# Kernel optimization log

Measured on AMD Instinct MI355X. Metric: run time of the kernel, lower is better.

The kernel has to match this reference:

```python
import jax, jax.numpy as jnp
import numpy as np

N = 150000   # nodes
E = 600000   # edges
F_IN = 32    # node features
H = 128      # hidden_channels == MLP_neurons
G = 2048     # graphs in batch


def setup_inputs() -> dict:
    key = jax.random.key(0)
    ks = iter(jax.random.split(key, 40))
    inp = {}
    inp['x'] = jax.random.normal(next(ks), (N, F_IN), dtype=jnp.float32)
    inp['edge_index'] = jax.random.randint(next(ks), (2, E), 0, N)
    inp['batch'] = jnp.sort(jax.random.randint(next(ks), (N,), 0, G))
    # GINConv MLPs: Linear(in,H) ReLU Linear(H,H) ReLU Linear(H,H)
    for i, f_in in enumerate([F_IN, H, H]):
        s1 = 1.0 / np.sqrt(f_in)
        s2 = 1.0 / np.sqrt(H)
        inp[f'c{i}_w1'] = jax.random.uniform(next(ks), (f_in, H), minval=-s1, maxval=s1)
        inp[f'c{i}_b1'] = jnp.zeros((H,), jnp.float32)
        inp[f'c{i}_w2'] = jax.random.uniform(next(ks), (H, H), minval=-s2, maxval=s2)
        inp[f'c{i}_b2'] = jnp.zeros((H,), jnp.float32)
        inp[f'c{i}_w3'] = jax.random.uniform(next(ks), (H, H), minval=-s2, maxval=s2)
        inp[f'c{i}_b3'] = jnp.zeros((H,), jnp.float32)
    s = 1.0 / np.sqrt(H)
    inp['fc0_w'] = jax.random.uniform(next(ks), (H, H), minval=-s, maxval=s)
    inp['fc0_b'] = jnp.zeros((H,), jnp.float32)
    inp['fc1_w'] = jax.random.uniform(next(ks), (H, H), minval=-s, maxval=s)
    inp['fc1_b'] = jnp.zeros((H,), jnp.float32)
    inp['out_w'] = jax.random.uniform(next(ks), (H, 2), minval=-s, maxval=s)
    inp['out_b'] = jnp.zeros((2,), jnp.float32)
    return inp


def _gin_layer(x, edge_index, w1, b1, w2, b2, w3, b3):
    # GINConv with eps=0: h = MLP(x + sum_{j in N(i)} x_j)
    agg = jax.ops.segment_sum(x[edge_index[0]], edge_index[1], num_segments=N)
    h = x + agg
    h = jax.nn.relu(h @ w1 + b1)
    h = jax.nn.relu(h @ w2 + b2)
    h = h @ w3 + b3
    return jax.nn.relu(h)  # outer .relu() in forward


def reference(x, edge_index, batch,
              c0_w1, c0_b1, c0_w2, c0_b2, c0_w3, c0_b3,
              c1_w1, c1_b1, c1_w2, c1_b2, c1_w3, c1_b3,
              c2_w1, c2_b1, c2_w2, c2_b2, c2_w3, c2_b3,
              fc0_w, fc0_b, fc1_w, fc1_b, out_w, out_b):
    h = _gin_layer(x, edge_index, c0_w1, c0_b1, c0_w2, c0_b2, c0_w3, c0_b3)
    h = _gin_layer(h, edge_index, c1_w1, c1_b1, c1_w2, c1_b2, c1_w3, c1_b3)
    h = _gin_layer(h, edge_index, c2_w1, c2_b1, c2_w2, c2_b2, c2_w3, c2_b3)
    # global_mean_pool over graph ids
    sums = jax.ops.segment_sum(h, batch, num_segments=G)            # [G,H]
    cnts = jax.ops.segment_sum(jnp.ones((N,), h.dtype), batch, num_segments=G)
    g = sums / jnp.maximum(cnts, 1.0)[:, None]
    # classifier head (dropout is identity at inference)
    g = jax.nn.relu(g @ fc0_w + fc0_b)
    g = jax.nn.relu(g @ fc1_w + fc1_b)
    return g @ out_w + out_b  # [G,2]
```

## Files before the change

kernel.cpp:

```cpp
#include <hip/hip_runtime.h>
#include <hip/hip_bf16.h>

#define NN 150000
#define EE 600000
#define F_IN 32
#define HD 128
#define GG 2048
#define CAP 28
#define NP 150016

typedef __attribute__((ext_vector_type(8))) short bf16x8;
typedef __attribute__((ext_vector_type(4))) float f32x4;
typedef __attribute__((address_space(1))) const void g1void;
typedef __attribute__((address_space(3))) void l3void;

__device__ inline void split_bf16(float v, unsigned short& hi, unsigned short& lo) {
    __hip_bfloat16 h = __float2bfloat16(v);
    float hv = __bfloat162float(h);
    __hip_bfloat16 l = __float2bfloat16(v - hv);
    hi = *reinterpret_cast<unsigned short*>(&h);
    lo = *reinterpret_cast<unsigned short*>(&l);
}
__device__ inline unsigned short bf16_hi(float v) {
    __hip_bfloat16 h = __float2bfloat16(v);
    return *reinterpret_cast<unsigned short*>(&h);
}
__device__ inline float bf2f(unsigned short u) {
    union { unsigned int i; float f; } c;
    c.i = ((unsigned int)u) << 16;
    return c.f;
}

__global__ void init_zero(int* __restrict__ cnt_node, float* __restrict__ pooled) {
    int i = blockIdx.x * blockDim.x + threadIdx.x;
    if (i < NN) cnt_node[i] = 0;
    if (i < GG * HD) pooled[i] = 0.f;
}

__global__ void build_graph(const int* __restrict__ ei,
                            int* __restrict__ cnt_node,
                            int* __restrict__ bucket) {
    int e = blockIdx.x * blockDim.x + threadIdx.x;
    if (e >= EE) return;
    int src = ei[e];
    int dst = ei[EE + e];
    int slot = atomicAdd(&cnt_node[dst], 1);
    if (slot < CAP) bucket[dst * CAP + slot] = src;
}

struct PrepDesc { const float* src; unsigned short* dhi; unsigned short* dlo; int K; };
struct PrepArgs { PrepDesc d[9]; };

__global__ void prep_weights(PrepArgs pa) {
    PrepDesc de = pa.d[blockIdx.y];
    int total = de.K * HD;
    int KS = de.K >> 5;
    for (int idx = blockIdx.x * blockDim.x + threadIdx.x; idx < total;
         idx += gridDim.x * blockDim.x) {
        int k = idx / HD, h = idx - (idx / HD) * HD;
        unsigned short hi, lo;
        split_bf16(de.src[idx], hi, lo);
        int nt = h >> 4, m = h & 15;
        int ks = k >> 5, quad = (k >> 3) & 3, e = k & 7;
        int lane = quad * 16 + m;
        int pidx = ((nt * KS + ks) * 64 + lane) * 8 + e;
        de.dhi[pidx] = hi;
        de.dlo[pidx] = lo;
    }
}

template <int KS>
__device__ inline void stage_slice(const unsigned short* __restrict__ wh,
                                   const unsigned short* __restrict__ wl,
                                   int nt, unsigned short* dst, int wave, int lane) {
    if (KS == 4) {
        const unsigned short* gh = wh + nt * 2048 + wave * 512 + lane * 8;
        const unsigned short* gl = wl + nt * 2048 + wave * 512 + lane * 8;
        __builtin_amdgcn_global_load_lds((g1void*)gh, (l3void*)(dst + wave * 512), 16, 0, 0);
        __builtin_amdgcn_global_load_lds((g1void*)gl, (l3void*)(dst + 2048 + wave * 512), 16, 0, 0);
    } else {
        if (wave < 2) {
            const unsigned short* g = (wave == 0 ? wh : wl) + nt * 512 + lane * 8;
            __builtin_amdgcn_global_load_lds((g1void*)g, (l3void*)(dst + wave * 512), 16, 0, 0);
        }
    }
}

template <int K_IN, bool BF16IN, bool POOL>
__launch_bounds__(256, 2)
__global__ void gin_layer(const void* __restrict__ hin_,
                          const int* __restrict__ cnt_node,
                          const int* __restrict__ bucket,
                          const unsigned short* __restrict__ w1h, const unsigned short* __restrict__ w1l,
                          const float* __restrict__ b1,
                          const unsigned short* __restrict__ w2h, const unsigned short* __restrict__ w2l,
                          const float* __restrict__ b2,
                          const unsigned short* __restrict__ w3h, const unsigned short* __restrict__ w3l,
                          const float* __restrict__ b3,
                          unsigned short* __restrict__ out,
                          const int* __restrict__ batch,
                          float* __restrict__ pooled) {
    constexpr int KS1 = K_IN / 32;
    constexpr int UN = BF16IN ? 4 : (KS1 == 1 ? 8 : 2);
    __shared__ unsigned int shp[4][2][16][128];
    __shared__ unsigned short ldsW[2][4096];

    const int wave = threadIdx.x >> 6;
    const int lane = threadIdx.x & 63;
    const int m = lane & 15;
    const int quad = lane >> 4;
    const int nodeBase = blockIdx.x * 128 + wave * 32;

    const float* hf = (const float*)hin_;
    const unsigned short* hb = (const unsigned short*)hin_;

    bf16x8 ah[2][KS1], al[2][KS1];
#pragma unroll
    for (int s = 0; s < 2; s++) {
        int node = nodeBase + s * 16 + m;
        node = node < NN ? node : NN - 1;
        float ag[KS1][8];
        if (BF16IN) {
            const unsigned short* rs = hb + (size_t)node * K_IN + quad * 8;
#pragma unroll
            for (int ks = 0; ks < KS1; ks++) {
                bf16x8 v = *(const bf16x8*)(rs + ks * 32);
#pragma unroll
                for (int e = 0; e < 8; e++) ag[ks][e] = bf2f((unsigned short)v[e]);
            }
        } else {
            const float* rs = hf + (size_t)node * K_IN + quad * 8;
#pragma unroll
            for (int ks = 0; ks < KS1; ks++) {
                float4 v0 = *(const float4*)(rs + ks * 32);
                float4 v1 = *(const float4*)(rs + ks * 32 + 4);
                ag[ks][0] = v0.x; ag[ks][1] = v0.y; ag[ks][2] = v0.z; ag[ks][3] = v0.w;
                ag[ks][4] = v1.x; ag[ks][5] = v1.y; ag[ks][6] = v1.z; ag[ks][7] = v1.w;
            }
        }
        int cnt = cnt_node[node];
        cnt = cnt < CAP ? cnt : CAP;
        const int* b = bucket + (size_t)node * CAP;
        int i = 0;
        if (BF16IN) {
            for (; i + UN <= cnt; i += UN) {
                bf16x8 v[UN][KS1];
#pragma unroll
                for (int j = 0; j < UN; j++) {
                    const unsigned short* r = hb + (size_t)b[i + j] * K_IN + quad * 8;
#pragma unroll
                    for (int ks = 0; ks < KS1; ks++)
                        v[j][ks] = *(const bf16x8*)(r + ks * 32);
                }
#pragma unroll
                for (int ks = 0; ks < KS1; ks++)
#pragma unroll
                    for (int e = 0; e < 8; e++) {
                        float t01 = bf2f((unsigned short)v[0][ks][e]) +
                                    bf2f((unsigned short)v[1][ks][e]);
                        float t23 = bf2f((unsigned short)v[2][ks][e]) +
                                    bf2f((unsigned short)v[3][ks][e]);
                        ag[ks][e] += t01 + t23;
                    }
            }
            for (; i < cnt; i++) {
                const unsigned short* r = hb + (size_t)b[i] * K_IN + quad * 8;
#pragma unroll
                for (int ks = 0; ks < KS1; ks++) {
                    bf16x8 v = *(const bf16x8*)(r + ks * 32);
#pragma unroll
                    for (int e = 0; e < 8; e++) ag[ks][e] += bf2f((unsigned short)v[e]);
                }
            }
        } else {
            for (; i + UN <= cnt; i += UN) {
                float4 v0[UN][KS1], v1[UN][KS1];
#pragma unroll
                for (int j = 0; j < UN; j++) {
                    const float* r = hf + (size_t)b[i + j] * K_IN + quad * 8;
#pragma unroll
                    for (int ks = 0; ks < KS1; ks++) {
                        v0[j][ks] = *(const float4*)(r + ks * 32);
                        v1[j][ks] = *(const float4*)(r + ks * 32 + 4);
                    }
                }
#pragma unroll
                for (int ks = 0; ks < KS1; ks++) {
#pragma unroll
                    for (int e = 0; e < 4; e++) {
                        float s01 = (&v0[0][ks].x)[e] + (&v0[1][ks].x)[e];
                        float s23 = (&v0[2][ks].x)[e] + (&v0[3][ks].x)[e];
                        if (UN == 8) {
                            s01 += (&v0[4][ks].x)[e] + (&v0[5][ks].x)[e];
                            s23 += (&v0[6][ks].x)[e] + (&v0[7][ks].x)[e];
                        }
                        ag[ks][e] += s01 + s23;
                    }
#pragma unroll
                    for (int e = 0; e < 4; e++) {
                        float s01 = (&v1[0][ks].x)[e] + (&v1[1][ks].x)[e];
                        float s23 = (&v1[2][ks].x)[e] + (&v1[3][ks].x)[e];
                        if (UN == 8) {
                            s01 += (&v1[4][ks].x)[e] + (&v1[5][ks].x)[e];
                            s23 += (&v1[6][ks].x)[e] + (&v1[7][ks].x)[e];
                        }
                        ag[ks][e + 4] += s01 + s23;
                    }
                }
            }
            for (; i < cnt; i++) {
                const float* r = hf + (size_t)b[i] * K_IN + quad * 8;
#pragma unroll
                for (int ks = 0; ks < KS1; ks++) {
                    float4 v0 = *(const float4*)(r + ks * 32);
                    float4 v1 = *(const float4*)(r + ks * 32 + 4);
                    ag[ks][0] += v0.x; ag[ks][1] += v0.y; ag[ks][2] += v0.z; ag[ks][3] += v0.w;
                    ag[ks][4] += v1.x; ag[ks][5] += v1.y; ag[ks][6] += v1.z; ag[ks][7] += v1.w;
                }
            }
        }
#pragma unroll
        for (int ks = 0; ks < KS1; ks++) {
            bf16x8 vh, vl;
#pragma unroll
            for (int e = 0; e < 8; e++) {
                unsigned short hi, lo;
                split_bf16(ag[ks][e], hi, lo);
                vh[e] = (short)hi;
                vl[e] = (short)lo;
            }
            ah[s][ks] = vh;
            al[s][ks] = vl;
        }
    }

    bf16x8 a2h[2][4], a2l[2][4];
    const int fxm = (m & 7) << 2;

    stage_slice<KS1>(w1h, w1l, 0, ldsW[0], wave, lane);
    __syncthreads();
#pragma unroll 1
    for (int nt = 0; nt < 8; nt++) {
        int cur = nt & 1;
        if (nt < 7) stage_slice<KS1>(w1h, w1l, nt + 1, ldsW[cur ^ 1], wave, lane);
        bf16x8 bh[KS1], bl[KS1];
#pragma unroll
        for (int ks = 0; ks < KS1; ks++) {
            bh[ks] = *(const bf16x8*)&ldsW[cur][(ks * 64 + lane) * 8];
            bl[ks] = *(const bf16x8*)&ldsW[cur][KS1 * 512 + (ks * 64 + lane) * 8];
        }
        f32x4 c0 = {0.f, 0.f, 0.f, 0.f};
        f32x4 c1 = {0.f, 0.f, 0.f, 0.f};
#pragma unroll
        for (int ks = 0; ks < KS1; ks++) {
            c0 = __builtin_amdgcn_mfma_f32_16x16x32_bf16(ah[0][ks], bh[ks], c0, 0, 0, 0);
            c1 = __builtin_amdgcn_mfma_f32_16x16x32_bf16(ah[1][ks], bh[ks], c1, 0, 0, 0);
            c0 = __builtin_amdgcn_mfma_f32_16x16x32_bf16(al[0][ks], bh[ks], c0, 0, 0, 0);
            c1 = __builtin_amdgcn_mfma_f32_16x16x32_bf16(al[1][ks], bh[ks], c1, 0, 0, 0);
            c0 = __builtin_amdgcn_mfma_f32_16x16x32_bf16(ah[0][ks], bl[ks], c0, 0, 0, 0);
            c1 = __builtin_amdgcn_mfma_f32_16x16x32_bf16(ah[1][ks], bl[ks], c1, 0, 0, 0);
        }
        float bj = b1[nt * 16 + m];
#pragma unroll
        for (int r = 0; r < 4; r++) {
            int row = quad * 4 + r;
            int col = (nt * 16 + m) ^ ((row & 7) << 2);
            unsigned short hi, lo;
            split_bf16(fmaxf(c0[r] + bj, 0.f), hi, lo);
            shp[wave][0][row][col] = (unsigned int)hi | ((unsigned int)lo << 16);
            split_bf16(fmaxf(c1[r] + bj, 0.f), hi, lo);
            shp[wave][1][row][col] = (unsigned int)hi | ((unsigned int)lo << 16);
        }
        __syncthreads();
    }
    stage_slice<4>(w2h, w2l, 0, ldsW[0], wave, lane);
#pragma unroll
    for (int s = 0; s < 2; s++)
#pragma unroll
        for (int ks = 0; ks < 4; ks++) {
            const unsigned int* rowp = &shp[wave][s][m][0];
            int base = ks * 32 + quad * 8;
            uint4 wa = *(const uint4*)&rowp[base ^ fxm];
            uint4 wb = *(const uint4*)&rowp[(base + 4) ^ fxm];
            union { unsigned int u[4]; bf16x8 v; } ch, cl;
            ch.u[0] = __builtin_amdgcn_perm(wa.y, wa.x, 0x05040100u);
            ch.u[1] = __builtin_amdgcn_perm(wa.w, wa.z, 0x05040100u);
            ch.u[2] = __builtin_amdgcn_perm(wb.y, wb.x, 0x05040100u);
            ch.u[3] = __builtin_amdgcn_perm(wb.w, wb.z, 0x05040100u);
            cl.u[0] = __builtin_amdgcn_perm(wa.y, wa.x, 0x07060302u);
            cl.u[1] = __builtin_amdgcn_perm(wa.w, wa.z, 0x07060302u);
            cl.u[2] = __builtin_amdgcn_perm(wb.y, wb.x, 0x07060302u);
            cl.u[3] = __builtin_amdgcn_perm(wb.w, wb.z, 0x07060302u);
            a2h[s][ks] = ch.v;
            a2l[s][ks] = cl.v;
        }
    __syncthreads();

#pragma unroll 1
    for (int nt = 0; nt < 8; nt++) {
        int cur = nt & 1;
        if (nt < 7) stage_slice<4>(w2h, w2l, nt + 1, ldsW[cur ^ 1], wave, lane);
        bf16x8 bh[4], bl[4];
#pragma unroll
        for (int ks = 0; ks < 4; ks++) {
            bh[ks] = *(const bf16x8*)&ldsW[cur][(ks * 64 + lane) * 8];
            bl[ks] = *(const bf16x8*)&ldsW[cur][2048 + (ks * 64 + lane) * 8];
        }
        f32x4 c0 = {0.f, 0.f, 0.f, 0.f};
        f32x4 c1 = {0.f, 0.f, 0.f, 0.f};
#pragma unroll
        for (int ks = 0; ks < 4; ks++) {
            c0 = __builtin_amdgcn_mfma_f32_16x16x32_bf16(a2h[0][ks], bh[ks], c0, 0, 0, 0);
            c1 = __builtin_amdgcn_mfma_f32_16x16x32_bf16(a2h[1][ks], bh[ks], c1, 0, 0, 0);
            c0 = __builtin_amdgcn_mfma_f32_16x16x32_bf16(a2l[0][ks], bh[ks], c0, 0, 0, 0);
            c1 = __builtin_amdgcn_mfma_f32_16x16x32_bf16(a2l[1][ks], bh[ks], c1, 0, 0, 0);
            c0 = __builtin_amdgcn_mfma_f32_16x16x32_bf16(a2h[0][ks], bl[ks], c0, 0, 0, 0);
            c1 = __builtin_amdgcn_mfma_f32_16x16x32_bf16(a2h[1][ks], bl[ks], c1, 0, 0, 0);
        }
        float bj = b2[nt * 16 + m];
#pragma unroll
        for (int r = 0; r < 4; r++) {
            int row = quad * 4 + r;
            int col = (nt * 16 + m) ^ ((row & 7) << 2);
            unsigned short hi, lo;
            split_bf16(fmaxf(c0[r] + bj, 0.f), hi, lo);
            shp[wave][0][row][col] = (unsigned int)hi | ((unsigned int)lo << 16);
            split_bf16(fmaxf(c1[r] + bj, 0.f), hi, lo);
            shp[wave][1][row][col] = (unsigned int)hi | ((unsigned int)lo << 16);
        }
        __syncthreads();
    }
    stage_slice<4>(w3h, w3l, 0, ldsW[0], wave, lane);
#pragma unroll
    for (int s = 0; s < 2; s++)
#pragma unroll
        for (int ks = 0; ks < 4; ks++) {
            const unsigned int* rowp = &shp[wave][s][m][0];
            int base = ks * 32 + quad * 8;
            uint4 wa = *(const uint4*)&rowp[base ^ fxm];
            uint4 wb = *(const uint4*)&rowp[(base + 4) ^ fxm];
            union { unsigned int u[4]; bf16x8 v; } ch, cl;
            ch.u[0] = __builtin_amdgcn_perm(wa.y, wa.x, 0x05040100u);
            ch.u[1] = __builtin_amdgcn_perm(wa.w, wa.z, 0x05040100u);
            ch.u[2] = __builtin_amdgcn_perm(wb.y, wb.x, 0x05040100u);
            ch.u[3] = __builtin_amdgcn_perm(wb.w, wb.z, 0x05040100u);
            cl.u[0] = __builtin_amdgcn_perm(wa.y, wa.x, 0x07060302u);
            cl.u[1] = __builtin_amdgcn_perm(wa.w, wa.z, 0x07060302u);
            cl.u[2] = __builtin_amdgcn_perm(wb.y, wb.x, 0x07060302u);
            cl.u[3] = __builtin_amdgcn_perm(wb.w, wb.z, 0x07060302u);
            a2h[s][ks] = ch.v;
            a2l[s][ks] = cl.v;
        }
    __syncthreads();

#pragma unroll 1
    for (int nt = 0; nt < 8; nt++) {
        int cur = nt & 1;
        if (nt < 7) stage_slice<4>(w3h, w3l, nt + 1, ldsW[cur ^ 1], wave, lane);
        bf16x8 bh[4], bl[4];
#pragma unroll
        for (int ks = 0; ks < 4; ks++) {
            bh[ks] = *(const bf16x8*)&ldsW[cur][(ks * 64 + lane) * 8];
            bl[ks] = *(const bf16x8*)&ldsW[cur][2048 + (ks * 64 + lane) * 8];
        }
        f32x4 c0 = {0.f, 0.f, 0.f, 0.f};
        f32x4 c1 = {0.f, 0.f, 0.f, 0.f};
#pragma unroll
        for (int ks = 0; ks < 4; ks++) {
            c0 = __builtin_amdgcn_mfma_f32_16x16x32_bf16(a2h[0][ks], bh[ks], c0, 0, 0, 0);
            c1 = __builtin_amdgcn_mfma_f32_16x16x32_bf16(a2h[1][ks], bh[ks], c1, 0, 0, 0);
            c0 = __builtin_amdgcn_mfma_f32_16x16x32_bf16(a2l[0][ks], bh[ks], c0, 0, 0, 0);
            c1 = __builtin_amdgcn_mfma_f32_16x16x32_bf16(a2l[1][ks], bh[ks], c1, 0, 0, 0);
            c0 = __builtin_amdgcn_mfma_f32_16x16x32_bf16(a2h[0][ks], bl[ks], c0, 0, 0, 0);
            c1 = __builtin_amdgcn_mfma_f32_16x16x32_bf16(a2h[1][ks], bl[ks], c1, 0, 0, 0);
        }
        float bj = b3[nt * 16 + m];
        if (POOL) {
            float* shf0 = (float*)&shp[wave][0][0][0];
            float* shf1 = (float*)&shp[wave][1][0][0];
#pragma unroll
            for (int r = 0; r < 4; r++) {
                int row = quad * 4 + r;
                int col = (nt * 16 + m) ^ ((row & 7) << 2);
                shf0[row * 128 + col] = fmaxf(c0[r] + bj, 0.f);
                shf1[row * 128 + col] = fmaxf(c1[r] + bj, 0.f);
            }
        } else {
            unsigned short* t0 = (unsigned short*)&shp[wave][0][0][0];
            unsigned short* t1 = (unsigned short*)&shp[wave][1][0][0];
#pragma unroll
            for (int r = 0; r < 4; r++) {
                int row = quad * 4 + r;
                int hh = nt * 16 + m;
                int w2 = (hh >> 1) ^ ((row & 7) << 2);
                t0[row * 256 + w2 * 2 + (hh & 1)] = bf16_hi(fmaxf(c0[r] + bj, 0.f));
                t1[row * 256 + w2 * 2 + (hh & 1)] = bf16_hi(fmaxf(c1[r] + bj, 0.f));
            }
        }
        __syncthreads();
    }

    if (POOL) {
#pragma unroll
        for (int h = 0; h < 2; h++) {
            float* shf = (float*)&shp[wave][h][0][0];
            int c0i = lane * 2;
            float run0 = 0.f, run1 = 0.f;
            int gp = -1;
            for (int rrow = 0; rrow < 16; rrow++) {
                int node = nodeBase + h * 16 + rrow;
                if (node >= NN) break;
                int g = batch[node];
                float2 xv = *(const float2*)&shf[rrow * 128 + (c0i ^ ((rrow & 7) << 2))];
                if (g != gp) {
                    if (gp >= 0) {
                        atomicAdd(&pooled[(size_t)gp * HD + c0i + 0], run0);
                        atomicAdd(&pooled[(size_t)gp * HD + c0i + 1], run1);
                    }
                    run0 = xv.x; run1 = xv.y; gp = g;
                } else {
                    run0 += xv.x; run1 += xv.y;
                }
            }
            if (gp >= 0) {
                atomicAdd(&pooled[(size_t)gp * HD + c0i + 0], run0);
                atomicAdd(&pooled[(size_t)gp * HD + c0i + 1], run1);
            }
        }
    } else {
#pragma unroll
        for (int s = 0; s < 2; s++) {
            unsigned short* sh16 = (unsigned short*)&shp[wave][s][0][0];
#pragma unroll
            for (int io = 0; io < 4; io++) {
                int row16 = io * 4 + quad;
                int wbase = (m * 4) ^ ((row16 & 7) << 2);
                int n2 = nodeBase + s * 16 + row16;
                bf16x8 v = *(const bf16x8*)&sh16[row16 * 256 + wbase * 2];
                if (n2 < NN) *(bf16x8*)&out[(size_t)n2 * HD + m * 8] = v;
            }
        }
    }
}

__device__ inline int lb_batch(const int* __restrict__ batch, int key) {
    int lo = 0, hi = NN;
    while (lo < hi) {
        int mid = (lo + hi) >> 1;
        if (batch[mid] < key) lo = mid + 1; else hi = mid;
    }
    return lo;
}

__launch_bounds__(128)
__global__ void head(const float* __restrict__ pooled, const int* __restrict__ batch,
                     const float* __restrict__ fc0_w, const float* __restrict__ fc0_b,
                     const float* __restrict__ fc1_w, const float* __restrict__ fc1_b,
                     const float* __restrict__ out_w, const float* __restrict__ out_b,
                     float* __restrict__ out) {
    int g = blockIdx.x;
    int j = threadIdx.x;
    __shared__ float s0[HD];
    __shared__ float s1[HD];
    int c = lb_batch(batch, g + 1) - lb_batch(batch, g);
    float cf = (float)(c > 1 ? c : 1);
    s0[j] = pooled[(size_t)g * HD + j] / cf;
    __syncthreads();

    float acc = fc0_b[j];
    for (int k = 0; k < HD; k += 4) {
        float4 hv = *(const float4*)&s0[k];
        acc = fmaf(hv.x, fc0_w[(k + 0) * HD + j], acc);
        acc = fmaf(hv.y, fc0_w[(k + 1) * HD + j], acc);
        acc = fmaf(hv.z, fc0_w[(k + 2) * HD + j], acc);
        acc = fmaf(hv.w, fc0_w[(k + 3) * HD + j], acc);
    }
    s1[j] = fmaxf(acc, 0.0f);
    __syncthreads();

    acc = fc1_b[j];
    for (int k = 0; k < HD; k += 4) {
        float4 hv = *(const float4*)&s1[k];
        acc = fmaf(hv.x, fc1_w[(k + 0) * HD + j], acc);
        acc = fmaf(hv.y, fc1_w[(k + 1) * HD + j], acc);
        acc = fmaf(hv.z, fc1_w[(k + 2) * HD + j], acc);
        acc = fmaf(hv.w, fc1_w[(k + 3) * HD + j], acc);
    }
    float v = fmaxf(acc, 0.0f);

    float p0 = v * out_w[j * 2 + 0];
    float p1 = v * out_w[j * 2 + 1];
    __syncthreads();
    s0[j] = p0;
    s1[j] = p1;
    __syncthreads();
    for (int off = 64; off >= 1; off >>= 1) {
        if (j < off) {
            s0[j] += s0[j + off];
            s1[j] += s1[j + off];
        }
        __syncthreads();
    }
    if (j == 0) {
        out[(size_t)g * 2 + 0] = s0[0] + out_b[0];
        out[(size_t)g * 2 + 1] = s1[0] + out_b[1];
    }
}

extern "C" void kernel_launch(void* const* d_in, const int* in_sizes, int n_in,
                              void* d_out, int out_size, void* d_ws, size_t ws_size,
                              hipStream_t stream) {
    const float* x     = (const float*)d_in[0];
    const int*   ei    = (const int*)d_in[1];
    const int*   batch = (const int*)d_in[2];
    const float* cw[3][6];
    for (int i = 0; i < 3; i++)
        for (int k = 0; k < 6; k++) cw[i][k] = (const float*)d_in[3 + 6 * i + k];
    const float* fc0_w = (const float*)d_in[21];
    const float* fc0_b = (const float*)d_in[22];
    const float* fc1_w = (const float*)d_in[23];
    const float* fc1_b = (const float*)d_in[24];
    const float* out_w = (const float*)d_in[25];
    const float* out_b = (const float*)d_in[26];
    float* out = (float*)d_out;

    char* ws = (char*)d_ws;
    size_t off = 0;
    auto carve = [&](size_t bytes) {
        void* p = ws + off;
        off += (bytes + 255) & ~(size_t)255;
        return p;
    };
    int*   cnt_node = (int*)carve((size_t)NN * 4);
    float* pooled   = (float*)carve((size_t)GG * HD * 4);
    int*   bucket   = (int*)carve((size_t)NN * CAP * 4);
    unsigned short* hA = (unsigned short*)carve((size_t)NP * HD * 2);
    unsigned short* hB = (unsigned short*)carve((size_t)NP * HD * 2);
    unsigned short* wHi[9];
    unsigned short* wLo[9];
    int wK[9] = {F_IN, HD, HD, HD, HD, HD, HD, HD, HD};
    for (int i = 0; i < 9; i++) {
        wHi[i] = (unsigned short*)carve((size_t)wK[i] * HD * 2);
        wLo[i] = (unsigned short*)carve((size_t)wK[i] * HD * 2);
    }
    (void)ws_size;

    init_zero<<<(GG * HD + 255) / 256, 256, 0, stream>>>(cnt_node, pooled);
    build_graph<<<(EE + 255) / 256, 256, 0, stream>>>(ei, cnt_node, bucket);

    PrepArgs pa;
    for (int l = 0; l < 3; l++)
        for (int s = 0; s < 3; s++) {
            int i = l * 3 + s;
            pa.d[i].src = cw[l][2 * s];
            pa.d[i].dhi = wHi[i];
            pa.d[i].dlo = wLo[i];
            pa.d[i].K = wK[i];
        }
    prep_weights<<<dim3(16, 9), 256, 0, stream>>>(pa);

    const int blocks = NP / 128;

    gin_layer<F_IN, false, false><<<blocks, 256, 0, stream>>>(x, cnt_node, bucket,
        wHi[0], wLo[0], cw[0][1], wHi[1], wLo[1], cw[0][3], wHi[2], wLo[2], cw[0][5],
        hA, batch, pooled);
    gin_layer<HD, true, false><<<blocks, 256, 0, stream>>>(hA, cnt_node, bucket,
        wHi[3], wLo[3], cw[1][1], wHi[4], wLo[4], cw[1][3], wHi[5], wLo[5], cw[1][5],
        hB, batch, pooled);
    gin_layer<HD, true, true><<<blocks, 256, 0, stream>>>(hB, cnt_node, bucket,
        wHi[6], wLo[6], cw[2][1], wHi[7], wLo[7], cw[2][3], wHi[8], wLo[8], cw[2][5],
        nullptr, batch, pooled);

    head<<<GG, 128, 0, stream>>>(pooled, batch, fc0_w, fc0_b, fc1_w, fc1_b, out_w, out_b, out);
}
```

Before: 474.6 us.

## Interleave neighbor gathers for both node halves and prefetch first weight slice earlier

The bf16 aggregation path now walks the neighbor lists of both 16-node halves together, two neighbors per step, using predicated loads that fall back to the node itself, so more independent gathers are in flight at once. The first W1 slice is staged into LDS before the gather so its load overlaps with aggregation. The fp32 path is specialised to KS1==1 with 8-way unrolling. The price is wasted loads when the two halves have different degrees, plus higher register pressure.

```diff
diff --git a/kernel.cpp b/kernel.cpp
--- a/kernel.cpp
+++ b/kernel.cpp
@@ -101,7 +101,6 @@
                           const int* __restrict__ batch,
                           float* __restrict__ pooled) {
     constexpr int KS1 = K_IN / 32;
-    constexpr int UN = BF16IN ? 4 : (KS1 == 1 ? 8 : 2);
     __shared__ unsigned int shp[4][2][16][128];
     __shared__ unsigned short ldsW[2][4096];
 
@@ -114,130 +113,128 @@
     const float* hf = (const float*)hin_;
     const unsigned short* hb = (const unsigned short*)hin_;
 
-    bf16x8 ah[2][KS1], al[2][KS1];
-#pragma unroll
-    for (int s = 0; s < 2; s++) {
-        int node = nodeBase + s * 16 + m;
-        node = node < NN ? node : NN - 1;
-        float ag[KS1][8];
-        if (BF16IN) {
-            const unsigned short* rs = hb + (size_t)node * K_IN + quad * 8;
+    stage_slice<KS1>(w1h, w1l, 0, ldsW[0], wave, lane);
+
+    float ag2[2][KS1][8];
+    if (BF16IN) {
+        int node0 = nodeBase + m;       node0 = node0 < NN ? node0 : NN - 1;
+        int node1 = nodeBase + 16 + m;  node1 = node1 < NN ? node1 : NN - 1;
+        const unsigned short* rs0 = hb + (size_t)node0 * K_IN + quad * 8;
+        const unsigned short* rs1 = hb + (size_t)node1 * K_IN + quad * 8;
+#pragma unroll
+        for (int ks = 0; ks < KS1; ks++) {
+            bf16x8 v0 = *(const bf16x8*)(rs0 + ks * 32);
+            bf16x8 v1 = *(const bf16x8*)(rs1 + ks * 32);
+#pragma unroll
+            for (int e = 0; e < 8; e++) {
+                ag2[0][ks][e] = bf2f((unsigned short)v0[e]);
+                ag2[1][ks][e] = bf2f((unsigned short)v1[e]);
+            }
+        }
+        int cnt0 = cnt_node[node0]; cnt0 = cnt0 < CAP ? cnt0 : CAP;
+        int cnt1 = cnt_node[node1]; cnt1 = cnt1 < CAP ? cnt1 : CAP;
+        const int* b0 = bucket + (size_t)node0 * CAP;
+        const int* b1p = bucket + (size_t)node1 * CAP;
+        int cmax = cnt0 > cnt1 ? cnt0 : cnt1;
+#pragma unroll 1
+        for (int i = 0; i < cmax; i += 2) {
+            bool v0a = i < cnt0, v0b = i + 1 < cnt0;
+            bool v1a = i < cnt1, v1b = i + 1 < cnt1;
+            int t0a = b0[i], t0b = b0[i + 1];
+            int t1a = b1p[i], t1b = b1p[i + 1];
+            int j0a = v0a ? t0a : node0;
+            int j0b = v0b ? t0b : node0;
+            int j1a = v1a ? t1a : node1;
+            int j1b = v1b ? t1b : node1;
+            const unsigned short* r0a = hb + (size_t)j0a * K_IN + quad * 8;
+            const unsigned short* r0b = hb + (size_t)j0b * K_IN + quad * 8;
+            const unsigned short* r1a = hb + (size_t)j1a * K_IN + quad * 8;
+            const unsigned short* r1b = hb + (size_t)j1b * K_IN + quad * 8;
+            bf16x8 w0a[KS1], w0b[KS1], w1a[KS1], w1b[KS1];
 #pragma unroll
             for (int ks = 0; ks < KS1; ks++) {
-                bf16x8 v = *(const bf16x8*)(rs + ks * 32);
-#pragma unroll
-                for (int e = 0; e < 8; e++) ag[ks][e] = bf2f((unsigned short)v[e]);
-            }
-        } else {
+                w0a[ks] = *(const bf16x8*)(r0a + ks * 32);
+                w0b[ks] = *(const bf16x8*)(r0b + ks * 32);
+                w1a[ks] = *(const bf16x8*)(r1a + ks * 32);
+                w1b[ks] = *(const bf16x8*)(r1b + ks * 32);
+            }
+#pragma unroll
+            for (int ks = 0; ks < KS1; ks++)
+#pragma unroll
+                for (int e = 0; e < 8; e++) {
+                    float x0a = v0a ? bf2f((unsigned short)w0a[ks][e]) : 0.f;
+                    float x0b = v0b ? bf2f((unsigned short)w0b[ks][e]) : 0.f;
+                    float x1a = v1a ? bf2f((unsigned short)w1a[ks][e]) : 0.f;
+                    float x1b = v1b ? bf2f((unsigned short)w1b[ks][e]) : 0.f;
+                    ag2[0][ks][e] += x0a + x0b;
+                    ag2[1][ks][e] += x1a + x1b;
+                }
+        }
+    } else {
+#pragma unroll
+        for (int s = 0; s < 2; s++) {
+            int node = nodeBase + s * 16 + m;
+            node = node < NN ? node : NN - 1;
             const float* rs = hf + (size_t)node * K_IN + quad * 8;
-#pragma unroll
-            for (int ks = 0; ks < KS1; ks++) {
-                float4 v0 = *(const float4*)(rs + ks * 32);
-                float4 v1 = *(const float4*)(rs + ks * 32 + 4);
-                ag[ks][0] = v0.x; ag[ks][1] = v0.y; ag[ks][2] = v0.z; ag[ks][3] = v0.w;
-                ag[ks][4] = v1.x; ag[ks][5] = v1.y; ag[ks][6] = v1.z; ag[ks][7] = v1.w;
-            }
-        }
-        int cnt = cnt_node[node];
-        cnt = cnt < CAP ? cnt : CAP;
-        const int* b = bucket + (size_t)node * CAP;
-        int i = 0;
-        if (BF16IN) {
-            for (; i + UN <= cnt; i += UN) {
-                bf16x8 v[UN][KS1];
-#pragma unroll
-                for (int j = 0; j < UN; j++) {
-                    const unsigned short* r = hb + (size_t)b[i + j] * K_IN + quad * 8;
-#pragma unroll
-                    for (int ks = 0; ks < KS1; ks++)
-                        v[j][ks] = *(const bf16x8*)(r + ks * 32);
+            float4 v0 = *(const float4*)rs;
+            float4 v1 = *(const float4*)(rs + 4);
+            ag2[s][0][0] = v0.x; ag2[s][0][1] = v0.y; ag2[s][0][2] = v0.z; ag2[s][0][3] = v0.w;
+            ag2[s][0][4] = v1.x; ag2[s][0][5] = v1.y; ag2[s][0][6] = v1.z; ag2[s][0][7] = v1.w;
+            int cnt = cnt_node[node];
+            cnt = cnt < CAP ? cnt : CAP;
+            const int* b = bucket + (size_t)node * CAP;
+            int i = 0;
+            for (; i + 8 <= cnt; i += 8) {
+                float4 a[8], c[8];
+#pragma unroll
+                for (int j = 0; j < 8; j++) {
+                    const float* r = hf + (size_t)b[i + j] * K_IN + quad * 8;
+                    a[j] = *(const float4*)r;
+                    c[j] = *(const float4*)(r + 4);
                 }
 #pragma unroll
-                for (int ks = 0; ks < KS1; ks++)
-#pragma unroll
-                    for (int e = 0; e < 8; e++) {
-                        float t01 = bf2f((unsigned short)v[0][ks][e]) +
-                                    bf2f((unsigned short)v[1][ks][e]);
-                        float t23 = bf2f((unsigned short)v[2][ks][e]) +
-                                    bf2f((unsigned short)v[3][ks][e]);
-                        ag[ks][e] += t01 + t23;
-                    }
-            }
-            for (; i < cnt; i++) {
-                const unsigned short* r = hb + (size_t)b[i] * K_IN + quad * 8;
-#pragma unroll
-                for (int ks = 0; ks < KS1; ks++) {
-                    bf16x8 v = *(const bf16x8*)(r + ks * 32);
-#pragma unroll
-                    for (int e = 0; e < 8; e++) ag[ks][e] += bf2f((unsigned short)v[e]);
+                for (int e = 0; e < 4; e++) {
+                    float s01 = (&a[0].x)[e] + (&a[1].x)[e] + (&a[4].x)[e] + (&a[5].x)[e];
+                    float s23 = (&a[2].x)[e] + (&a[3].x)[e] + (&a[6].x)[e] + (&a[7].x)[e];
+                    ag2[s][0][e] += s01 + s23;
                 }
-            }
-        } else {
-            for (; i + UN <= cnt; i += UN) {
-                float4 v0[UN][KS1], v1[UN][KS1];
-#pragma unroll
-                for (int j = 0; j < UN; j++) {
-                    const float* r = hf + (size_t)b[i + j] * K_IN + quad * 8;
-#pragma unroll
-                    for (int ks = 0; ks < KS1; ks++) {
-                        v0[j][ks] = *(const float4*)(r + ks * 32);
-                        v1[j][ks] = *(const float4*)(r + ks * 32 + 4);
-                    }
-                }
-#pragma unroll
-                for (int ks = 0; ks < KS1; ks++) {
-#pragma unroll
-                    for (int e = 0; e < 4; e++) {
-                        float s01 = (&v0[0][ks].x)[e] + (&v0[1][ks].x)[e];
-                        float s23 = (&v0[2][ks].x)[e] + (&v0[3][ks].x)[e];
-                        if (UN == 8) {
-                            s01 += (&v0[4][ks].x)[e] + (&v0[5][ks].x)[e];
-                            s23 += (&v0[6][ks].x)[e] + (&v0[7][ks].x)[e];
-                        }
-                        ag[ks][e] += s01 + s23;
-                    }
-#pragma unroll
-                    for (int e = 0; e < 4; e++) {
-                        float s01 = (&v1[0][ks].x)[e] + (&v1[1][ks].x)[e];
-                        float s23 = (&v1[2][ks].x)[e] + (&v1[3][ks].x)[e];
-                        if (UN == 8) {
-                            s01 += (&v1[4][ks].x)[e] + (&v1[5][ks].x)[e];
-                            s23 += (&v1[6][ks].x)[e] + (&v1[7][ks].x)[e];
-                        }
-                        ag[ks][e + 4] += s01 + s23;
-                    }
+#pragma unroll
+                for (int e = 0; e < 4; e++) {
+                    float s01 = (&c[0].x)[e] + (&c[1].x)[e] + (&c[4].x)[e] + (&c[5].x)[e];
+                    float s23 = (&c[2].x)[e] + (&c[3].x)[e] + (&c[6].x)[e] + (&c[7].x)[e];
+                    ag2[s][0][e + 4] += s01 + s23;
                 }
             }
             for (; i < cnt; i++) {
                 const float* r = hf + (size_t)b[i] * K_IN + quad * 8;
-#pragma unroll
-                for (int ks = 0; ks < KS1; ks++) {
-                    float4 v0 = *(const float4*)(r + ks * 32);
-                    float4 v1 = *(const float4*)(r + ks * 32 + 4);
-                    ag[ks][0] += v0.x; ag[ks][1] += v0.y; ag[ks][2] += v0.z; ag[ks][3] += v0.w;
-                    ag[ks][4] += v1.x; ag[ks][5] += v1.y; ag[ks][6] += v1.z; ag[ks][7] += v1.w;
-                }
-            }
-        }
+                float4 v0i = *(const float4*)r;
+                float4 v1i = *(const float4*)(r + 4);
+                ag2[s][0][0] += v0i.x; ag2[s][0][1] += v0i.y; ag2[s][0][2] += v0i.z; ag2[s][0][3] += v0i.w;
+                ag2[s][0][4] += v1i.x; ag2[s][0][5] += v1i.y; ag2[s][0][6] += v1i.z; ag2[s][0][7] += v1i.w;
+            }
+        }
+    }
+
+    bf16x8 ah[2][KS1], al[2][KS1];
+#pragma unroll
+    for (int s = 0; s < 2; s++)
 #pragma unroll
         for (int ks = 0; ks < KS1; ks++) {
             bf16x8 vh, vl;
 #pragma unroll
             for (int e = 0; e < 8; e++) {
                 unsigned short hi, lo;
-                split_bf16(ag[ks][e], hi, lo);
+                split_bf16(ag2[s][ks][e], hi, lo);
                 vh[e] = (short)hi;
                 vl[e] = (short)lo;
             }
             ah[s][ks] = vh;
             al[s][ks] = vl;
         }
-    }
 
     bf16x8 a2h[2][4], a2l[2][4];
     const int fxm = (m & 7) << 2;
 
-    stage_slice<KS1>(w1h, w1l, 0, ldsW[0], wave, lane);
     __syncthreads();
 #pragma unroll 1
     for (int nt = 0; nt < 8; nt++) {
```

New measurement: 553.7 us. 1.17x slower.
